# Optimization experiments

Measured on AMD Instinct MI355X. Metric: run time of the kernel, lower is better.

The kernel has to match this reference:

```python
import jax, jax.numpy as jnp
import numpy as np

NUM_HEADS = 16
D_MODEL = 1024


def setup_inputs() -> dict:
    key = jax.random.key(0)
    ks = jax.random.split(key, 12)
    B, S, D = 2, 2048, D_MODEL
    scale = 1.0 / np.sqrt(D)
    inp = {
        "query": jax.random.normal(ks[0], (B, S, D), dtype=jnp.float32),
        "key": jax.random.normal(ks[1], (B, S, D), dtype=jnp.float32),
        "value": jax.random.normal(ks[2], (B, S, D), dtype=jnp.float32),
        "mask": jax.random.randint(ks[3], (B, S, S), 0, 2, dtype=jnp.int32),
        # four Linear(d_model, d_model) layers: torch layout W [out, in], y = x @ W.T + b
        "Wq": jax.random.normal(ks[4], (D, D), dtype=jnp.float32) * scale,
        "bq": jnp.zeros((D,), dtype=jnp.float32),
        "Wk": jax.random.normal(ks[5], (D, D), dtype=jnp.float32) * scale,
        "bk": jnp.zeros((D,), dtype=jnp.float32),
        "Wv": jax.random.normal(ks[6], (D, D), dtype=jnp.float32) * scale,
        "bv": jnp.zeros((D,), dtype=jnp.float32),
        "Wo": jax.random.normal(ks[7], (D, D), dtype=jnp.float32) * scale,
        "bo": jnp.zeros((D,), dtype=jnp.float32),
    }
    return inp


def reference(query, key, value, mask, Wq, bq, Wk, bk, Wv, bv, Wo, bo):
    B, S, D = query.shape
    H = NUM_HEADS
    dk = D // H

    def split_heads(x):  # [B,S,D] -> [B,H,S,dk]
        return x.reshape(B, S, H, dk).transpose(0, 2, 1, 3)

    q = split_heads(query @ Wq.T + bq)
    k = split_heads(key @ Wk.T + bk)
    v = split_heads(value @ Wv.T + bv)

    # naive full-score attention, faithful to the original
    scores = jnp.einsum("bhqd,bhkd->bhqk", q, k) / jnp.sqrt(jnp.asarray(dk, q.dtype))
    scores = jnp.where(mask[:, None, :, :] == 0, jnp.asarray(-1e9, scores.dtype), scores)
    probs = jax.nn.softmax(scores, axis=-1)
    attn = jnp.einsum("bhqk,bhkd->bhqd", probs, v)  # [B,H,S,dk]

    out = attn.transpose(0, 2, 1, 3).reshape(B, S, D)
    return out @ Wo.T + bo
```

## Files before the change

kernel.cpp:

```cpp
#include <hip/hip_runtime.h>
#include <hip/hip_bf16.h>

#define NH 16
#define DK 64
#define SEQ 2048
#define DMODEL 1024
#define BATCH 2
#define MROWS (BATCH * SEQ)

using bf16x8 = __attribute__((ext_vector_type(8))) short;
using f32x4  = __attribute__((ext_vector_type(4))) float;

#define NEGI (-1e30f)
#define QSCALE 0.18033688f

static __device__ __forceinline__ unsigned short f2bf(float x) {
  unsigned u = __builtin_bit_cast(unsigned, x);
  u += 0x7fffu + ((u >> 16) & 1u);
  return (unsigned short)(u >> 16);
}
static __device__ __forceinline__ float bf2f(unsigned short h) {
  unsigned u = ((unsigned)h) << 16;
  return __builtin_bit_cast(float, u);
}
static __device__ __forceinline__ unsigned cvtpk(float a, float b) {
  unsigned r;
  asm("v_cvt_pk_bf16_f32 %0, %1, %2" : "=v"(r) : "v"(a), "v"(b));
  return r;
}

__global__ __launch_bounds__(256) void convert3(const float* __restrict__ s0,
                                                const float* __restrict__ s1,
                                                const float* __restrict__ s2,
                                                unsigned short* __restrict__ d0,
                                                unsigned short* __restrict__ d1,
                                                unsigned short* __restrict__ d2,
                                                long n8, int blkseg) {
  int seg = blockIdx.x / blkseg;
  int ib  = blockIdx.x % blkseg;
  const float* s = seg == 0 ? s0 : (seg == 1 ? s1 : s2);
  unsigned short* d = seg == 0 ? d0 : (seg == 1 ? d1 : d2);
  long i0 = (long)ib * blockDim.x + threadIdx.x;
  long stride = (long)blkseg * blockDim.x;
  for (long i = i0; i < n8; i += stride) {
    const float* p = s + i * 8;
    float4 a = *(const float4*)(p);
    float4 b = *(const float4*)(p + 4);
    bf16x8 v;
    v[0] = (short)f2bf(a.x); v[1] = (short)f2bf(a.y);
    v[2] = (short)f2bf(a.z); v[3] = (short)f2bf(a.w);
    v[4] = (short)f2bf(b.x); v[5] = (short)f2bf(b.y);
    v[6] = (short)f2bf(b.z); v[7] = (short)f2bf(b.w);
    *(bf16x8*)(d + i * 8) = v;
  }
}
__global__ __launch_bounds__(256) void convert4(const float* __restrict__ s0,
                                                const float* __restrict__ s1,
                                                const float* __restrict__ s2,
                                                const float* __restrict__ s3,
                                                unsigned short* __restrict__ d0,
                                                unsigned short* __restrict__ d1,
                                                unsigned short* __restrict__ d2,
                                                unsigned short* __restrict__ d3,
                                                long n8, int blkseg) {
  int seg = blockIdx.x / blkseg;
  int ib  = blockIdx.x % blkseg;
  const float* s = seg == 0 ? s0 : (seg == 1 ? s1 : (seg == 2 ? s2 : s3));
  unsigned short* d = seg == 0 ? d0 : (seg == 1 ? d1 : (seg == 2 ? d2 : d3));
  long i0 = (long)ib * blockDim.x + threadIdx.x;
  long stride = (long)blkseg * blockDim.x;
  for (long i = i0; i < n8; i += stride) {
    const float* p = s + i * 8;
    float4 a = *(const float4*)(p);
    float4 b = *(const float4*)(p + 4);
    bf16x8 v;
    v[0] = (short)f2bf(a.x); v[1] = (short)f2bf(a.y);
    v[2] = (short)f2bf(a.z); v[3] = (short)f2bf(a.w);
    v[4] = (short)f2bf(b.x); v[5] = (short)f2bf(b.y);
    v[6] = (short)f2bf(b.z); v[7] = (short)f2bf(b.w);
    *(bf16x8*)(d + i * 8) = v;
  }
}

__global__ __launch_bounds__(256) void pack_mask(const int* __restrict__ mask,
                                                 unsigned long long* __restrict__ pm,
                                                 int nwords) {
  int wid  = (blockIdx.x * blockDim.x + threadIdx.x) >> 6;
  int lane = threadIdx.x & 63;
  int nw   = (gridDim.x * blockDim.x) >> 6;
  for (int w = wid; w < nwords; w += nw) {
    int v = mask[(long)w * 64 + lane];
    unsigned long long b = __ballot(v != 0);
    if (lane == 0) pm[w] = b;
  }
}

#define BK 64
#define LDA2 72

static __device__ __forceinline__ void gemm_body(const unsigned short* __restrict__ A,
                                                 const unsigned short* __restrict__ W,
                                                 const unsigned short* __restrict__ bias,
                                                 void* __restrict__ Cv,
                                                 int mode, float cscale, int bid,
                                                 unsigned short* Al, unsigned short* Bl) {
  const int t    = threadIdx.x;
  const int lane = t & 63;
  const int w    = t >> 6;
  const int wm   = w >> 1, wn = w & 1;
  const int g    = lane >> 4, lr = lane & 15;
  const int nb   = bid & 7;
  const int mb   = bid >> 3;
  const long Abase = (long)mb * 128 * 1024;
  const long Wbase = (long)nb * 128 * 1024;

  f32x4 acc[4][4] = {};

  for (int kt = 0; kt < 1024; kt += BK) {
    __syncthreads();
#pragma unroll
    for (int q = 0; q < 4; ++q) {
      int id  = q * 256 + t;
      int row = id >> 3;
      int c8  = (id & 7) << 3;
      bf16x8 va = *(const bf16x8*)(A + Abase + (long)row * 1024 + kt + c8);
      bf16x8 vb = *(const bf16x8*)(W + Wbase + (long)row * 1024 + kt + c8);
      *(bf16x8*)(&Al[row * LDA2 + c8]) = va;
      *(bf16x8*)(&Bl[row * LDA2 + c8]) = vb;
    }
    __syncthreads();
#pragma unroll
    for (int kh = 0; kh < 2; ++kh) {
      bf16x8 af[4], bfr[4];
#pragma unroll
      for (int i = 0; i < 4; ++i) {
        af[i]  = *(const bf16x8*)(&Al[(wm * 64 + i * 16 + lr) * LDA2 + kh * 32 + g * 8]);
        bfr[i] = *(const bf16x8*)(&Bl[(wn * 64 + i * 16 + lr) * LDA2 + kh * 32 + g * 8]);
      }
#pragma unroll
      for (int i = 0; i < 4; ++i)
#pragma unroll
        for (int j = 0; j < 4; ++j)
          acc[i][j] = __builtin_amdgcn_mfma_f32_16x16x32_bf16(af[i], bfr[j], acc[i][j], 0, 0, 0);
    }
  }

#pragma unroll
  for (int j = 0; j < 4; ++j) {
    int n = nb * 128 + wn * 64 + j * 16 + lr;
    float bv = bf2f(bias[n]);
#pragma unroll
    for (int i = 0; i < 4; ++i) {
      int m0 = mb * 128 + wm * 64 + i * 16 + g * 4;
      float v0 = (acc[i][j][0] + bv) * cscale;
      float v1 = (acc[i][j][1] + bv) * cscale;
      float v2 = (acc[i][j][2] + bv) * cscale;
      float v3 = (acc[i][j][3] + bv) * cscale;
      if (mode == 2) {
        int b = m0 >> 11, s0 = m0 & (SEQ - 1);
        int h = n >> 6, d = n & (DK - 1);
        uint2 pk;
        pk.x = (unsigned)f2bf(v0) | ((unsigned)f2bf(v1) << 16);
        pk.y = (unsigned)f2bf(v2) | ((unsigned)f2bf(v3) << 16);
        *(uint2*)(&((unsigned short*)Cv)[((long)(b * NH + h) * DK + d) * SEQ + s0]) = pk;
      } else if (mode == 1) {
        int b = m0 >> 11, s0 = m0 & (SEQ - 1);
        int h = n >> 6, d = n & (DK - 1);
        unsigned short* p = &((unsigned short*)Cv)[(((long)(b * NH + h) * SEQ + s0) << 6) + d];
        p[0] = f2bf(v0); p[64] = f2bf(v1); p[128] = f2bf(v2); p[192] = f2bf(v3);
      } else {
        float* p = &((float*)Cv)[(long)m0 * DMODEL + n];
        p[0] = v0; p[DMODEL] = v1; p[2 * DMODEL] = v2; p[3 * DMODEL] = v3;
      }
    }
  }
}

__global__ __launch_bounds__(256) void qkv_proj(const unsigned short* __restrict__ Aq,
                                                const unsigned short* __restrict__ Ak,
                                                const unsigned short* __restrict__ Av,
                                                const unsigned short* __restrict__ Wq,
                                                const unsigned short* __restrict__ Wk,
                                                const unsigned short* __restrict__ Wv,
                                                const unsigned short* __restrict__ bq,
                                                const unsigned short* __restrict__ bk,
                                                const unsigned short* __restrict__ bv,
                                                unsigned short* __restrict__ Cq,
                                                unsigned short* __restrict__ Ck,
                                                unsigned short* __restrict__ Cv) {
  __shared__ unsigned short Al[128 * LDA2];
  __shared__ unsigned short Bl[128 * LDA2];
  int which = blockIdx.x >> 8;
  int bid   = blockIdx.x & 255;
  const unsigned short* A = which == 0 ? Aq : (which == 1 ? Ak : Av);
  const unsigned short* W = which == 0 ? Wq : (which == 1 ? Wk : Wv);
  const unsigned short* b = which == 0 ? bq : (which == 1 ? bk : bv);
  unsigned short* C = which == 0 ? Cq : (which == 1 ? Ck : Cv);
  int   mode  = which == 2 ? 2 : 1;
  float scale = which == 0 ? QSCALE : 1.0f;
  gemm_body(A, W, b, C, mode, scale, bid, Al, Bl);
}

__global__ __launch_bounds__(256) void gemm_out(const unsigned short* __restrict__ A,
                                                const unsigned short* __restrict__ W,
                                                const unsigned short* __restrict__ bias,
                                                float* __restrict__ C) {
  __shared__ unsigned short Al[128 * LDA2];
  __shared__ unsigned short Bl[128 * LDA2];
  gemm_body(A, W, bias, C, 0, 1.0f, blockIdx.x, Al, Bl);
}

#define KVB 64
#define LD 72

__global__ __launch_bounds__(256) void attn(const unsigned short* __restrict__ Q,
                                            const unsigned short* __restrict__ K,
                                            const unsigned short* __restrict__ VT,
                                            const unsigned long long* __restrict__ pm,
                                            unsigned short* __restrict__ O) {
  __shared__ unsigned short Kl[KVB * LD];
  __shared__ unsigned short Vt[DK * LD];
  __shared__ unsigned short Pl[4][32 * LD];
  const int t    = threadIdx.x;
  const int lane = t & 63;
  const int w    = t >> 6;
  const int g    = lane >> 4, lr = lane & 15;
  const int bh   = blockIdx.x & 31;
  const int qb   = blockIdx.x >> 5;
  const int b    = bh >> 4, h = bh & 15;
  const long base = (long)bh * SEQ * DK;
  const int q0   = qb * 128 + w * 32;

  bf16x8 qf[2][2];
#pragma unroll
  for (int qh = 0; qh < 2; ++qh) {
    const unsigned short* qp = Q + base + (long)(q0 + qh * 16 + lr) * DK;
    qf[qh][0] = *(const bf16x8*)(qp + g * 8);
    qf[qh][1] = *(const bf16x8*)(qp + 32 + g * 8);
  }
  float mrun[2] = {NEGI, NEGI}, lrun[2] = {0.f, 0.f};
  f32x4 o[2][4] = {};

  for (int kt = 0; kt < SEQ / KVB; ++kt) {
    const int kvbase = kt * KVB;
    __syncthreads();
#pragma unroll
    for (int p = 0; p < 2; ++p) {
      int id  = p * 256 + t;
      int row = id >> 3;
      int c8  = (id & 7) << 3;
      bf16x8 kv8 = *(const bf16x8*)(K + base + (long)(kvbase + row) * DK + c8);
      *(bf16x8*)(&Kl[row * LD + c8]) = kv8;
    }
#pragma unroll
    for (int p = 0; p < 2; ++p) {
      int id  = p * 256 + t;
      int row = id >> 3;
      int c8  = (id & 7) << 3;
      bf16x8 vv = *(const bf16x8*)(VT + base + (long)row * SEQ + kvbase + c8);
      *(bf16x8*)(&Vt[row * LD + c8]) = vv;
    }
    __syncthreads();

    f32x4 sc[2][4];
#pragma unroll
    for (int c = 0; c < 4; ++c) {
      bf16x8 kf0 = *(const bf16x8*)(&Kl[(c * 16 + lr) * LD + g * 8]);
      bf16x8 kf1 = *(const bf16x8*)(&Kl[(c * 16 + lr) * LD + 32 + g * 8]);
#pragma unroll
      for (int qh = 0; qh < 2; ++qh) {
        f32x4 a = {};
        a = __builtin_amdgcn_mfma_f32_16x16x32_bf16(kf0, qf[qh][0], a, 0, 0, 0);
        a = __builtin_amdgcn_mfma_f32_16x16x32_bf16(kf1, qf[qh][1], a, 0, 0, 0);
        sc[qh][c] = a;
      }
    }

    unsigned short* P = &Pl[w][0];
#pragma unroll
    for (int qh = 0; qh < 2; ++qh) {
      const unsigned long long mw = pm[((long)b * SEQ + q0 + qh * 16 + lr) * 32 + kt];
      float s[4][4];
      float mt = NEGI;
#pragma unroll
      for (int c = 0; c < 4; ++c)
#pragma unroll
        for (int r = 0; r < 4; ++r) {
          int kvi = c * 16 + g * 4 + r;
          float v = ((mw >> kvi) & 1ull) ? sc[qh][c][r] : -1e9f;
          s[c][r] = v;
          mt = fmaxf(mt, v);
        }
      mt = fmaxf(mt, __shfl_xor(mt, 16, 64));
      mt = fmaxf(mt, __shfl_xor(mt, 32, 64));

      int need = __any(mt > mrun[qh] + 5.0f);
      float mn = mrun[qh], corr = 1.0f;
      if (need) { mn = fmaxf(mrun[qh], mt); corr = __builtin_amdgcn_exp2f(mrun[qh] - mn); mrun[qh] = mn; }

      float pf[4][4];
      float rs = 0.f;
#pragma unroll
      for (int c = 0; c < 4; ++c)
#pragma unroll
        for (int r = 0; r < 4; ++r) {
          float p_ = __builtin_amdgcn_exp2f(s[c][r] - mn);
          pf[c][r] = p_;
          rs += p_;
        }
      rs += __shfl_xor(rs, 16, 64);
      rs += __shfl_xor(rs, 32, 64);

      if (need) {
        lrun[qh] = lrun[qh] * corr + rs;
#pragma unroll
        for (int r = 0; r < 4; ++r) {
          float cq = __shfl(corr, (lane >> 4) * 4 + r, 64);
#pragma unroll
          for (int dt = 0; dt < 4; ++dt) o[qh][dt][r] *= cq;
        }
      } else {
        lrun[qh] += rs;
      }

#pragma unroll
      for (int c = 0; c < 4; ++c) {
        uint2 pk;
        pk.x = cvtpk(pf[c][0], pf[c][1]);
        pk.y = cvtpk(pf[c][2], pf[c][3]);
        *(uint2*)(&P[(qh * 16 + lr) * LD + c * 16 + g * 4]) = pk;
      }
    }
    __syncthreads();
#pragma unroll
    for (int c32 = 0; c32 < 2; ++c32) {
      bf16x8 pf0 = *(const bf16x8*)(&P[lr * LD + c32 * 32 + g * 8]);
      bf16x8 pf1 = *(const bf16x8*)(&P[(16 + lr) * LD + c32 * 32 + g * 8]);
#pragma unroll
      for (int dt = 0; dt < 4; ++dt) {
        bf16x8 vf = *(const bf16x8*)(&Vt[(dt * 16 + lr) * LD + c32 * 32 + g * 8]);
        o[0][dt] = __builtin_amdgcn_mfma_f32_16x16x32_bf16(pf0, vf, o[0][dt], 0, 0, 0);
        o[1][dt] = __builtin_amdgcn_mfma_f32_16x16x32_bf16(pf1, vf, o[1][dt], 0, 0, 0);
      }
    }
  }
#pragma unroll
  for (int qh = 0; qh < 2; ++qh) {
    float inv = 1.0f / lrun[qh];
#pragma unroll
    for (int r = 0; r < 4; ++r) {
      float iq = __shfl(inv, (lane >> 4) * 4 + r, 64);
      int q = q0 + qh * 16 + g * 4 + r;
      unsigned short* op = O + ((long)(b * SEQ + q) * DMODEL) + h * DK;
#pragma unroll
      for (int dt = 0; dt < 4; ++dt) op[dt * 16 + lr] = f2bf(o[qh][dt][r] * iq);
    }
  }
}

extern "C" void kernel_launch(void* const* d_in, const int* in_sizes, int n_in,
                              void* d_out, int out_size, void* d_ws, size_t ws_size,
                              hipStream_t stream) {
  const int* maskp = (const int*)d_in[3];
  float* out = (float*)d_out;

  char* ws = (char*)d_ws;
  const long MB = 1 << 20;
  unsigned long long* pm = (unsigned long long*)ws;
  unsigned short* Qc  = (unsigned short*)(ws + 1 * MB);
  unsigned short* Kc  = (unsigned short*)(ws + 9 * MB);
  unsigned short* Vc  = (unsigned short*)(ws + 17 * MB);
  unsigned short* Wqc = (unsigned short*)(ws + 25 * MB);
  unsigned short* Wkc = (unsigned short*)(ws + 27 * MB);
  unsigned short* Wvc = (unsigned short*)(ws + 29 * MB);
  unsigned short* Woc = (unsigned short*)(ws + 31 * MB);
  unsigned short* bqc = (unsigned short*)(ws + 33 * MB);
  unsigned short* bkc = (unsigned short*)(ws + 33 * MB + 4096);
  unsigned short* bvc = (unsigned short*)(ws + 33 * MB + 8192);
  unsigned short* boc = (unsigned short*)(ws + 33 * MB + 12288);
  unsigned short* Qb  = (unsigned short*)(ws + 35 * MB);
  unsigned short* Kb  = (unsigned short*)(ws + 43 * MB);
  unsigned short* Vb  = (unsigned short*)(ws + 51 * MB);
  unsigned short* Ab  = (unsigned short*)(ws + 59 * MB);

  const long nQKV8 = (long)MROWS * DMODEL / 8;
  const long nW8   = (long)DMODEL * DMODEL / 8;
  convert3<<<1536, 256, 0, stream>>>((const float*)d_in[0], (const float*)d_in[1],
                                     (const float*)d_in[2], Qc, Kc, Vc, nQKV8, 512);
  convert4<<<512, 256, 0, stream>>>((const float*)d_in[4], (const float*)d_in[6],
                                    (const float*)d_in[8], (const float*)d_in[10],
                                    Wqc, Wkc, Wvc, Woc, nW8, 128);
  convert4<<<4, 256, 0, stream>>>((const float*)d_in[5], (const float*)d_in[7],
                                  (const float*)d_in[9], (const float*)d_in[11],
                                  bqc, bkc, bvc, boc, DMODEL / 8, 1);

  const int nwords = BATCH * SEQ * (SEQ / 64);
  pack_mask<<<512, 256, 0, stream>>>(maskp, pm, nwords);

  qkv_proj<<<768, 256, 0, stream>>>(Qc, Kc, Vc, Wqc, Wkc, Wvc,
                                    bqc, bkc, bvc, Qb, Kb, Vb);

  attn<<<BATCH * NH * (SEQ / 128), 256, 0, stream>>>(Qb, Kb, Vb, pm, Ab);

  gemm_out<<<256, 256, 0, stream>>>(Ab, Woc, boc, out);
}
```

Before: 196.1 us.

## Fuse fp32-to-bf16 conversion into GEMM tile loads and relax attention barrier

The standalone conversion kernels for the activations, weights and biases are removed. The GEMM body is templated so it reads fp32 global data directly and packs it to bf16 with v_cvt_pk_bf16_f32 while staging tiles into shared memory. This saves several launches and a full write-then-reread of bf16 copies, but each GEMM tile load now fetches twice as many bytes and repeats the conversion for every block that reuses the same tile. Separately, the block-wide barrier in the attention loop is replaced by an LDS wait plus a scheduling barrier, relying on the P tile being private to each wave.

```diff
diff --git a/kernel.cpp b/kernel.cpp
--- a/kernel.cpp
+++ b/kernel.cpp
@@ -19,67 +19,10 @@
   u += 0x7fffu + ((u >> 16) & 1u);
   return (unsigned short)(u >> 16);
 }
-static __device__ __forceinline__ float bf2f(unsigned short h) {
-  unsigned u = ((unsigned)h) << 16;
-  return __builtin_bit_cast(float, u);
-}
 static __device__ __forceinline__ unsigned cvtpk(float a, float b) {
   unsigned r;
   asm("v_cvt_pk_bf16_f32 %0, %1, %2" : "=v"(r) : "v"(a), "v"(b));
   return r;
-}
-
-__global__ __launch_bounds__(256) void convert3(const float* __restrict__ s0,
-                                                const float* __restrict__ s1,
-                                                const float* __restrict__ s2,
-                                                unsigned short* __restrict__ d0,
-                                                unsigned short* __restrict__ d1,
-                                                unsigned short* __restrict__ d2,
-                                                long n8, int blkseg) {
-  int seg = blockIdx.x / blkseg;
-  int ib  = blockIdx.x % blkseg;
-  const float* s = seg == 0 ? s0 : (seg == 1 ? s1 : s2);
-  unsigned short* d = seg == 0 ? d0 : (seg == 1 ? d1 : d2);
-  long i0 = (long)ib * blockDim.x + threadIdx.x;
-  long stride = (long)blkseg * blockDim.x;
-  for (long i = i0; i < n8; i += stride) {
-    const float* p = s + i * 8;
-    float4 a = *(const float4*)(p);
-    float4 b = *(const float4*)(p + 4);
-    bf16x8 v;
-    v[0] = (short)f2bf(a.x); v[1] = (short)f2bf(a.y);
-    v[2] = (short)f2bf(a.z); v[3] = (short)f2bf(a.w);
-    v[4] = (short)f2bf(b.x); v[5] = (short)f2bf(b.y);
-    v[6] = (short)f2bf(b.z); v[7] = (short)f2bf(b.w);
-    *(bf16x8*)(d + i * 8) = v;
-  }
-}
-__global__ __launch_bounds__(256) void convert4(const float* __restrict__ s0,
-                                                const float* __restrict__ s1,
-                                                const float* __restrict__ s2,
-                                                const float* __restrict__ s3,
-                                                unsigned short* __restrict__ d0,
-                                                unsigned short* __restrict__ d1,
-                                                unsigned short* __restrict__ d2,
-                                                unsigned short* __restrict__ d3,
-                                                long n8, int blkseg) {
-  int seg = blockIdx.x / blkseg;
-  int ib  = blockIdx.x % blkseg;
-  const float* s = seg == 0 ? s0 : (seg == 1 ? s1 : (seg == 2 ? s2 : s3));
-  unsigned short* d = seg == 0 ? d0 : (seg == 1 ? d1 : (seg == 2 ? d2 : d3));
-  long i0 = (long)ib * blockDim.x + threadIdx.x;
-  long stride = (long)blkseg * blockDim.x;
-  for (long i = i0; i < n8; i += stride) {
-    const float* p = s + i * 8;
-    float4 a = *(const float4*)(p);
-    float4 b = *(const float4*)(p + 4);
-    bf16x8 v;
-    v[0] = (short)f2bf(a.x); v[1] = (short)f2bf(a.y);
-    v[2] = (short)f2bf(a.z); v[3] = (short)f2bf(a.w);
-    v[4] = (short)f2bf(b.x); v[5] = (short)f2bf(b.y);
-    v[6] = (short)f2bf(b.z); v[7] = (short)f2bf(b.w);
-    *(bf16x8*)(d + i * 8) = v;
-  }
 }
 
 __global__ __launch_bounds__(256) void pack_mask(const int* __restrict__ mask,
@@ -98,9 +41,10 @@
 #define BK 64
 #define LDA2 72
 
-static __device__ __forceinline__ void gemm_body(const unsigned short* __restrict__ A,
-                                                 const unsigned short* __restrict__ W,
-                                                 const unsigned short* __restrict__ bias,
+template <int AF32, int WF32>
+static __device__ __forceinline__ void gemm_body(const void* __restrict__ Avp,
+                                                 const void* __restrict__ Wvp,
+                                                 const float* __restrict__ bias,
                                                  void* __restrict__ Cv,
                                                  int mode, float cscale, int bid,
                                                  unsigned short* Al, unsigned short* Bl) {
@@ -123,8 +67,25 @@
       int id  = q * 256 + t;
       int row = id >> 3;
       int c8  = (id & 7) << 3;
-      bf16x8 va = *(const bf16x8*)(A + Abase + (long)row * 1024 + kt + c8);
-      bf16x8 vb = *(const bf16x8*)(W + Wbase + (long)row * 1024 + kt + c8);
+      bf16x8 va, vb;
+      if (AF32) {
+        const float* ap = (const float*)Avp + Abase + (long)row * 1024 + kt + c8;
+        float4 x = *(const float4*)ap;
+        float4 y = *(const float4*)(ap + 4);
+        uint4 u = {cvtpk(x.x, x.y), cvtpk(x.z, x.w), cvtpk(y.x, y.y), cvtpk(y.z, y.w)};
+        va = __builtin_bit_cast(bf16x8, u);
+      } else {
+        va = *(const bf16x8*)((const unsigned short*)Avp + Abase + (long)row * 1024 + kt + c8);
+      }
+      if (WF32) {
+        const float* wp = (const float*)Wvp + Wbase + (long)row * 1024 + kt + c8;
+        float4 x = *(const float4*)wp;
+        float4 y = *(const float4*)(wp + 4);
+        uint4 u = {cvtpk(x.x, x.y), cvtpk(x.z, x.w), cvtpk(y.x, y.y), cvtpk(y.z, y.w)};
+        vb = __builtin_bit_cast(bf16x8, u);
+      } else {
+        vb = *(const bf16x8*)((const unsigned short*)Wvp + Wbase + (long)row * 1024 + kt + c8);
+      }
       *(bf16x8*)(&Al[row * LDA2 + c8]) = va;
       *(bf16x8*)(&Bl[row * LDA2 + c8]) = vb;
     }
@@ -148,7 +109,7 @@
 #pragma unroll
   for (int j = 0; j < 4; ++j) {
     int n = nb * 128 + wn * 64 + j * 16 + lr;
-    float bv = bf2f(bias[n]);
+    float bv = bias[n];
 #pragma unroll
     for (int i = 0; i < 4; ++i) {
       int m0 = mb * 128 + wm * 64 + i * 16 + g * 4;
@@ -176,15 +137,15 @@
   }
 }
 
-__global__ __launch_bounds__(256) void qkv_proj(const unsigned short* __restrict__ Aq,
-                                                const unsigned short* __restrict__ Ak,
-                                                const unsigned short* __restrict__ Av,
-                                                const unsigned short* __restrict__ Wq,
-                                                const unsigned short* __restrict__ Wk,
-                                                const unsigned short* __restrict__ Wv,
-                                                const unsigned short* __restrict__ bq,
-                                                const unsigned short* __restrict__ bk,
-                                                const unsigned short* __restrict__ bv,
+__global__ __launch_bounds__(256) void qkv_proj(const float* __restrict__ Aq,
+                                                const float* __restrict__ Ak,
+                                                const float* __restrict__ Av,
+                                                const float* __restrict__ Wq,
+                                                const float* __restrict__ Wk,
+                                                const float* __restrict__ Wv,
+                                                const float* __restrict__ bq,
+                                                const float* __restrict__ bk,
+                                                const float* __restrict__ bv,
                                                 unsigned short* __restrict__ Cq,
                                                 unsigned short* __restrict__ Ck,
                                                 unsigned short* __restrict__ Cv) {
@@ -192,22 +153,22 @@
   __shared__ unsigned short Bl[128 * LDA2];
   int which = blockIdx.x >> 8;
   int bid   = blockIdx.x & 255;
-  const unsigned short* A = which == 0 ? Aq : (which == 1 ? Ak : Av);
-  const unsigned short* W = which == 0 ? Wq : (which == 1 ? Wk : Wv);
-  const unsigned short* b = which == 0 ? bq : (which == 1 ? bk : bv);
+  const float* A = which == 0 ? Aq : (which == 1 ? Ak : Av);
+  const float* W = which == 0 ? Wq : (which == 1 ? Wk : Wv);
+  const float* b = which == 0 ? bq : (which == 1 ? bk : bv);
   unsigned short* C = which == 0 ? Cq : (which == 1 ? Ck : Cv);
   int   mode  = which == 2 ? 2 : 1;
   float scale = which == 0 ? QSCALE : 1.0f;
-  gemm_body(A, W, b, C, mode, scale, bid, Al, Bl);
+  gemm_body<1, 1>(A, W, b, C, mode, scale, bid, Al, Bl);
 }
 
 __global__ __launch_bounds__(256) void gemm_out(const unsigned short* __restrict__ A,
-                                                const unsigned short* __restrict__ W,
-                                                const unsigned short* __restrict__ bias,
+                                                const float* __restrict__ W,
+                                                const float* __restrict__ bias,
                                                 float* __restrict__ C) {
   __shared__ unsigned short Al[128 * LDA2];
   __shared__ unsigned short Bl[128 * LDA2];
-  gemm_body(A, W, bias, C, 0, 1.0f, blockIdx.x, Al, Bl);
+  gemm_body<0, 1>(A, W, bias, C, 0, 1.0f, blockIdx.x, Al, Bl);
 }
 
 #define KVB 64
@@ -331,7 +292,9 @@
         *(uint2*)(&P[(qh * 16 + lr) * LD + c * 16 + g * 4]) = pk;
       }
     }
-    __syncthreads();
+    asm volatile("s_waitcnt lgkmcnt(0)" ::: "memory");
+    __builtin_amdgcn_sched_barrier(0);
+
 #pragma unroll
     for (int c32 = 0; c32 < 2; ++c32) {
       bf16x8 pf0 = *(const bf16x8*)(&P[lr * LD + c32 * 32 + g * 8]);
@@ -343,6 +306,8 @@
         o[1][dt] = __builtin_amdgcn_mfma_f32_16x16x32_bf16(pf1, vf, o[1][dt], 0, 0, 0);
       }
     }
+    asm volatile("s_waitcnt lgkmcnt(0)" ::: "memory");
+    __builtin_amdgcn_sched_barrier(0);
   }
 #pragma unroll
   for (int qh = 0; qh < 2; ++qh) {
@@ -367,40 +332,24 @@
   char* ws = (char*)d_ws;
   const long MB = 1 << 20;
   unsigned long long* pm = (unsigned long long*)ws;
-  unsigned short* Qc  = (unsigned short*)(ws + 1 * MB);
-  unsigned short* Kc  = (unsigned short*)(ws + 9 * MB);
-  unsigned short* Vc  = (unsigned short*)(ws + 17 * MB);
-  unsigned short* Wqc = (unsigned short*)(ws + 25 * MB);
-  unsigned short* Wkc = (unsigned short*)(ws + 27 * MB);
-  unsigned short* Wvc = (unsigned short*)(ws + 29 * MB);
-  unsigned short* Woc = (unsigned short*)(ws + 31 * MB);
-  unsigned short* bqc = (unsigned short*)(ws + 33 * MB);
-  unsigned short* bkc = (unsigned short*)(ws + 33 * MB + 4096);
-  unsigned short* bvc = (unsigned short*)(ws + 33 * MB + 8192);
-  unsigned short* boc = (unsigned short*)(ws + 33 * MB + 12288);
   unsigned short* Qb  = (unsigned short*)(ws + 35 * MB);
   unsigned short* Kb  = (unsigned short*)(ws + 43 * MB);
   unsigned short* Vb  = (unsigned short*)(ws + 51 * MB);
   unsigned short* Ab  = (unsigned short*)(ws + 59 * MB);
 
-  const long nQKV8 = (long)MROWS * DMODEL / 8;
-  const long nW8   = (long)DMODEL * DMODEL / 8;
-  convert3<<<1536, 256, 0, stream>>>((const float*)d_in[0], (const float*)d_in[1],
-                                     (const float*)d_in[2], Qc, Kc, Vc, nQKV8, 512);
-  convert4<<<512, 256, 0, stream>>>((const float*)d_in[4], (const float*)d_in[6],
-                                    (const float*)d_in[8], (const float*)d_in[10],
-                                    Wqc, Wkc, Wvc, Woc, nW8, 128);
-  convert4<<<4, 256, 0, stream>>>((const float*)d_in[5], (const float*)d_in[7],
-                                  (const float*)d_in[9], (const float*)d_in[11],
-                                  bqc, bkc, bvc, boc, DMODEL / 8, 1);
-
   const int nwords = BATCH * SEQ * (SEQ / 64);
   pack_mask<<<512, 256, 0, stream>>>(maskp, pm, nwords);
 
-  qkv_proj<<<768, 256, 0, stream>>>(Qc, Kc, Vc, Wqc, Wkc, Wvc,
-                                    bqc, bkc, bvc, Qb, Kb, Vb);
+  qkv_proj<<<768, 256, 0, stream>>>((const float*)d_in[0], (const float*)d_in[1],
+                                    (const float*)d_in[2],
+                                    (const float*)d_in[4], (const float*)d_in[6],
+                                    (const float*)d_in[8],
+                                    (const float*)d_in[5], (const float*)d_in[7],
+                                    (const float*)d_in[9],
+                                    Qb, Kb, Vb);
 
   attn<<<BATCH * NH * (SEQ / 128), 256, 0, stream>>>(Qb, Kb, Vb, pm, Ab);
 
-  gemm_out<<<256, 256, 0, stream>>>(Ab, Woc, boc, out);
-}
+  gemm_out<<<256, 256, 0, stream>>>(Ab, (const float*)d_in[10],
+                                    (const float*)d_in[11], out);
+}
```

Result: slower. 209.8 us (+7.0%).
